# Optimization experiments

Hardware: AMD Instinct MI355X
Metric: run time of the kernel (lower is better)

The kernel has to match this reference:

```python
import jax, jax.numpy as jnp
import numpy as np

CLASS_NUM = 20
C_FEAT = 256
STRIDE = 16
ROI = 7
SCALE = 1.0 / 16.0
TOPK = 300
NMS_THR = 0.7
SCORE_THR = 0.5
SAMPLES = 2  # nearest samples per bin edge in roi_pool


def _conv(x, W, b, stride, padding):
    y = jax.lax.conv_general_dilated(x, W, (stride, stride), padding,
                                     dimension_numbers=('NCHW', 'OIHW', 'NCHW'))
    return y + b[None, :, None, None]


def _pairwise_iou(boxes):
    x1, y1, x2, y2 = boxes[:, 0], boxes[:, 1], boxes[:, 2], boxes[:, 3]
    area = jnp.maximum(x2 - x1, 0.) * jnp.maximum(y2 - y1, 0.)
    ix1 = jnp.maximum(x1[:, None], x1[None, :])
    iy1 = jnp.maximum(y1[:, None], y1[None, :])
    ix2 = jnp.minimum(x2[:, None], x2[None, :])
    iy2 = jnp.minimum(y2[:, None], y2[None, :])
    inter = jnp.maximum(ix2 - ix1, 0.) * jnp.maximum(iy2 - iy1, 0.)
    return inter / jnp.maximum(area[:, None] + area[None, :] - inter, 1e-6)


def _nms(boxes, scores, valid, thr):
    # fixed-size greedy NMS: returns boolean keep mask aligned with input order
    K = boxes.shape[0]
    order = jnp.argsort(-scores)
    b = boxes[order]
    v = valid[order]
    iou = _pairwise_iou(b)  # [K,K]
    idx = jnp.arange(K)

    def body(i, keep):
        k = keep[i] & v[i]
        suppress = (iou[i] > thr) & (idx > i) & k
        return keep & (~suppress)

    keep = jax.lax.fori_loop(0, K, body, v)
    return jnp.zeros((K,), bool).at[order].set(keep)


def _roi_pool(f, boxes):
    # f: [C,H,W] feature map; boxes: [K,4] in image coords.
    # Max pool over ROI x SAMPLES nearest-neighbor samples per bin (jit-safe roi_pool).
    C, H, W = f.shape
    K = boxes.shape[0]
    b = boxes * SCALE
    frac = (jnp.arange(ROI)[:, None] + (jnp.arange(SAMPLES)[None, :] + 0.5) / SAMPLES).reshape(-1) / ROI
    xs = b[:, 0:1] + frac[None, :] * (b[:, 2:3] - b[:, 0:1])  # [K, ROI*S]
    ys = b[:, 1:2] + frac[None, :] * (b[:, 3:4] - b[:, 1:2])
    ix = jnp.clip(jnp.floor(xs), 0, W - 1).astype(jnp.int32)
    iy = jnp.clip(jnp.floor(ys), 0, H - 1).astype(jnp.int32)
    g = f[:, iy[:, :, None], ix[:, None, :]]  # [C,K,ROI*S,ROI*S]
    g = g.reshape(C, K, ROI, SAMPLES, ROI, SAMPLES)
    return g.max(axis=(3, 5)).transpose(1, 0, 2, 3)  # [K,C,ROI,ROI]


def setup_inputs() -> dict:
    key = jax.random.key(0)
    ks = jax.random.split(key, 12)
    img = 800
    x = jax.random.uniform(ks[0], (1, 3, img, img), jnp.float32)
    gt_boxes = jax.random.uniform(ks[1], (8, 5), jnp.float32) * img

    def w_(k, shape, fan_in):
        return jax.random.normal(k, shape, jnp.float32) * (1.0 / np.sqrt(fan_in))

    d_flat = ROI * ROI * C_FEAT
    return {
        'x': x, 'gt_boxes': gt_boxes,
        'W_feat': w_(ks[2], (C_FEAT, 3, STRIDE, STRIDE), 3 * STRIDE * STRIDE),
        'b_feat': jnp.zeros((C_FEAT,), jnp.float32),
        'W1': w_(ks[3], (C_FEAT, C_FEAT, 3, 3), C_FEAT * 9),
        'b1': jnp.zeros((C_FEAT,), jnp.float32),
        'Wc': w_(ks[4], (2, C_FEAT), C_FEAT),
        'bc': jnp.zeros((2,), jnp.float32),
        'Wb': w_(ks[5], (4, C_FEAT), C_FEAT),
        'bb': jnp.zeros((4,), jnp.float32),
        'fc1_w': w_(ks[6], (4096, d_flat), d_flat),
        'fc1_b': jnp.zeros((4096,), jnp.float32),
        'fc2_w': w_(ks[7], (4096, 4096), 4096),
        'fc2_b': jnp.zeros((4096,), jnp.float32),
        'cls_w': w_(ks[8], (CLASS_NUM + 1, 4096), 4096),
        'cls_b': jnp.zeros((CLASS_NUM + 1,), jnp.float32),
        'box_w': w_(ks[9], (4, 4096), 4096),
        'box_b': jnp.zeros((4,), jnp.float32),
        'w': 800, 'h': 800,
    }


def reference(x, gt_boxes, W_feat, b_feat, W1, b1, Wc, bc, Wb, bb,
              fc1_w, fc1_b, fc2_w, fc2_b, cls_w, cls_b, box_w, box_b, w, h):
    feature = _conv(x, W_feat, b_feat, STRIDE, 'VALID')          # [1,C,50,50]
    hmap = jax.nn.relu(_conv(feature, W1, b1, 1, 'SAME'))
    pre_labels = (jnp.einsum('nchw,oc->nhwo', hmap, Wc) + bc).reshape(-1, 2)
    pre_boxes = (jnp.einsum('nchw,oc->nhwo', hmap, Wb) + bb).reshape(-1, 4)
    logits = jax.nn.softmax(pre_labels, axis=-1)[:, 1]           # [2500]
    scores, idx = jax.lax.top_k(logits, TOPK)                    # fixed-size stand-in for score>thr select
    valid = scores > SCORE_THR
    pb = pre_boxes[idx]
    wf = jnp.float32(w)
    hf = jnp.float32(h)
    # box decode exactly as the original per-box loop (vectorized)
    x1 = jnp.maximum(pb[:, 2] - pb[:, 0] / 2, 0.)
    y1 = jnp.maximum(pb[:, 3] - pb[:, 1] / 2, 0.)
    x2 = jnp.minimum(pb[:, 2] + pb[:, 0], wf)
    y2 = jnp.minimum(pb[:, 3] + pb[:, 1], hf)
    boxes = jnp.stack([x1, y1, x2, y2], axis=-1)                 # [K,4]
    keep = _nms(boxes, scores, valid, NMS_THR)
    pooled = _roi_pool(feature[0], boxes)                        # [K,C,7,7]
    flat = pooled.reshape(TOPK, -1)
    h1 = jax.nn.relu(flat @ fc1_w.T + fc1_b)
    h2 = jax.nn.relu(h1 @ fc2_w.T + fc2_b)
    cls = h2 @ cls_w.T + cls_b                                   # [K,21]
    box = h2 @ box_w.T + box_b                                   # [K,4]
    out = jnp.where(keep[:, None], jnp.concatenate([cls, box], axis=-1), 0.)
    return out                                                   # [K,25]
```

## Files before the change

kernel.cpp:

```cpp
#include <hip/hip_runtime.h>
#include <hip/hip_bf16.h>
#include <math.h>

#define NPIX   2500
#define CFEAT  256
#define NTOP   300
#define DFLAT  12544
#define FCN    4096
#define FPSTRIDE 3328
#define KG1    392
#define KG2    128
#define MT     20

typedef _Float16 f16x8 __attribute__((ext_vector_type(8)));
typedef float    f32x4 __attribute__((ext_vector_type(4)));

static constexpr size_t OFF_FPAD  = 0;
static constexpr size_t OFF_SCORE = 0x5C0000;
static constexpr size_t OFF_PREB  = 0x5D0000;
static constexpr size_t OFF_KEEP  = 0x5E5000;
static constexpr size_t OFF_IX    = 0x5E6000;
static constexpr size_t OFF_IY    = 0x5EB000;
static constexpr size_t OFF_AFRAG = 0x600000;
static constexpr size_t OFF_H1F   = 0xE00000;
static constexpr size_t OFF_H2    = 0x1100000;
static constexpr size_t OFF_W1T   = 0x1600000;
static constexpr size_t OFF_PART  = 0x1900000;

__device__ inline float decode_dim(const void* p) {
    int iv = *(const int*)p;
    if (iv > 0 && iv < (1 << 20)) return (float)iv;
    return __int_as_float(iv);
}

__global__ void zero_fpad(float* __restrict__ fpad) {
    int i = blockIdx.x * 256 + threadIdx.x;
    if (i < 212992) *(float4*)(fpad + (size_t)i * 4) = make_float4(0.f, 0.f, 0.f, 0.f);
}

__global__ void __launch_bounds__(256)
patch_conv(const float* __restrict__ x, const float* __restrict__ Wf,
           const float* __restrict__ bf, float* __restrict__ fpad) {
    __shared__ float w[3072];
    int co0 = blockIdx.y * 4;
    for (int t = threadIdx.x; t < 3072; t += 256) w[t] = Wf[co0 * 768 + t];
    __syncthreads();
    int p = blockIdx.x * 256 + threadIdx.x;
    if (p >= NPIX) return;
    int py = p / 50, px = p % 50;
    float acc[4];
    #pragma unroll
    for (int c = 0; c < 4; ++c) acc[c] = bf[co0 + c];
    for (int ci = 0; ci < 3; ++ci) {
        const float* xp = x + ci * 640000 + (py * 16) * 800 + px * 16;
        #pragma unroll
        for (int ky = 0; ky < 16; ++ky) {
            const float* row = xp + ky * 800;
            #pragma unroll
            for (int kq = 0; kq < 4; ++kq) {
                float4 xv = *reinterpret_cast<const float4*>(row + kq * 4);
                int kb = ci * 256 + ky * 16 + kq * 4;
                #pragma unroll
                for (int c = 0; c < 4; ++c) {
                    const float* wc = w + c * 768 + kb;
                    acc[c] += xv.x * wc[0] + xv.y * wc[1] + xv.z * wc[2] + xv.w * wc[3];
                }
            }
        }
    }
    size_t o = (size_t)(py + 1) * 64 + (px + 1);
    #pragma unroll
    for (int c = 0; c < 4; ++c) fpad[(size_t)(co0 + c) * FPSTRIDE + o] = acc[c];
}

__global__ void transpose_w1(const float* __restrict__ W1, float* __restrict__ W1t) {
    int idx = blockIdx.x * 256 + threadIdx.x;
    if (idx >= 2304 * 256) return;
    int r = idx >> 8, co = idx & 255;
    W1t[idx] = W1[co * 2304 + r];
}

__global__ void __launch_bounds__(256)
conv3x3_part(const float* __restrict__ fpad, const float* __restrict__ W1t,
             float* __restrict__ cpart, int zci) {
    int co = threadIdx.x;
    int xb = blockIdx.x * 8;
    int y  = blockIdx.y;
    int z  = blockIdx.z;
    float acc[8];
    #pragma unroll
    for (int p = 0; p < 8; ++p) acc[p] = 0.0f;
    const float* fp = fpad + (size_t)(z * zci) * FPSTRIDE + (size_t)y * 64 + xb;
    const float* wp = W1t + (size_t)(z * zci) * 9 * 256 + co;
    #pragma unroll 2
    for (int ci = 0; ci < zci; ++ci) {
        float v[3][12];
        #pragma unroll
        for (int dy = 0; dy < 3; ++dy) {
            #pragma unroll
            for (int q = 0; q < 3; ++q) {
                float4 r4 = *(const float4*)(fp + dy * 64 + q * 4);
                v[dy][q * 4 + 0] = r4.x; v[dy][q * 4 + 1] = r4.y;
                v[dy][q * 4 + 2] = r4.z; v[dy][q * 4 + 3] = r4.w;
            }
        }
        float wv[9];
        #pragma unroll
        for (int k = 0; k < 9; ++k) wv[k] = wp[k * 256];
        #pragma unroll
        for (int dy = 0; dy < 3; ++dy)
            #pragma unroll
            for (int dx = 0; dx < 3; ++dx) {
                float wvv = wv[dy * 3 + dx];
                #pragma unroll
                for (int p = 0; p < 8; ++p)
                    acc[p] += v[dy][p + dx] * wvv;
            }
        fp += FPSTRIDE;
        wp += 9 * 256;
    }
    size_t base = (size_t)z * (NPIX * 256) + (size_t)(y * 50 + xb) * 256 + co;
    #pragma unroll
    for (int p = 0; p < 8; ++p)
        if (xb + p < 50) cpart[base + (size_t)p * 256] = acc[p];
}

__global__ void __launch_bounds__(256)
reducehead_k(const float* __restrict__ cpart, const float* __restrict__ b1,
             const float* __restrict__ Wc, const float* __restrict__ bc,
             const float* __restrict__ Wb, const float* __restrict__ bb,
             float* __restrict__ score, float* __restrict__ preb, int zs) {
    int lane = threadIdx.x & 63;
    int p = blockIdx.x * 4 + (threadIdx.x >> 6);
    if (p >= NPIX) return;
    size_t off = (size_t)p * 256 + lane * 4;
    float4 h = *(const float4*)(cpart + off);
    for (int z = 1; z < zs; ++z) {
        float4 v = *(const float4*)(cpart + (size_t)z * (NPIX * 256) + off);
        h.x += v.x; h.y += v.y; h.z += v.z; h.w += v.w;
    }
    float4 b = *(const float4*)(b1 + lane * 4);
    h.x = fmaxf(h.x + b.x, 0.f); h.y = fmaxf(h.y + b.y, 0.f);
    h.z = fmaxf(h.z + b.z, 0.f); h.w = fmaxf(h.w + b.w, 0.f);
    float4 c0 = *(const float4*)(Wc + lane * 4);
    float4 c1 = *(const float4*)(Wc + 256 + lane * 4);
    float4 w0 = *(const float4*)(Wb + lane * 4);
    float4 w1 = *(const float4*)(Wb + 256 + lane * 4);
    float4 w2 = *(const float4*)(Wb + 512 + lane * 4);
    float4 w3 = *(const float4*)(Wb + 768 + lane * 4);
    float s[6];
    s[0] = h.x*c0.x + h.y*c0.y + h.z*c0.z + h.w*c0.w;
    s[1] = h.x*c1.x + h.y*c1.y + h.z*c1.z + h.w*c1.w;
    s[2] = h.x*w0.x + h.y*w0.y + h.z*w0.z + h.w*w0.w;
    s[3] = h.x*w1.x + h.y*w1.y + h.z*w1.z + h.w*w1.w;
    s[4] = h.x*w2.x + h.y*w2.y + h.z*w2.z + h.w*w2.w;
    s[5] = h.x*w3.x + h.y*w3.y + h.z*w3.z + h.w*w3.w;
    #pragma unroll
    for (int o = 1; o < 64; o <<= 1) {
        #pragma unroll
        for (int q = 0; q < 6; ++q) s[q] += __shfl_xor(s[q], o, 64);
    }
    if (lane == 0) {
        float s0 = s[0] + bc[0], s1 = s[1] + bc[1];
        float m = fmaxf(s0, s1);
        float e0 = expf(s0 - m), e1 = expf(s1 - m);
        score[p] = e1 / (e0 + e1);
        preb[p * 4 + 0] = s[2] + bb[0];
        preb[p * 4 + 1] = s[3] + bb[1];
        preb[p * 4 + 2] = s[4] + bb[2];
        preb[p * 4 + 3] = s[5] + bb[3];
    }
}

__global__ void __launch_bounds__(1024)
topknms_k(const float* __restrict__ score, const float* __restrict__ preb,
          const void* wp_, const void* hp_, int* __restrict__ keep,
          int* __restrict__ ixb, int* __restrict__ iyb) {
    __shared__ unsigned long long KEYS[NPIX];
    __shared__ unsigned int hist[256];
    __shared__ int sh_digit, sh_newr, cnt;
    __shared__ unsigned long long SEL[NTOP];
    __shared__ unsigned long long SORT[NTOP];
    __shared__ float X1[320], Y1[320], X2[320], Y2[320], AR[320];
    __shared__ unsigned long long MASK[320][5];
    __shared__ unsigned long long KEEPW[5];
    int tid = threadIdx.x;
    int lane = tid & 63;
    int w = tid >> 6;

    for (int e = tid; e < NPIX; e += 1024) {
        unsigned sb = __float_as_uint(score[e]);
        KEYS[e] = ((unsigned long long)sb << 32) | (unsigned)(~e);
    }
    if (tid == 0) cnt = 0;
    __syncthreads();

    unsigned long long P = 0ull, M = 0ull;
    int r = NTOP;
    for (int pass = 0; pass < 8; ++pass) {
        int shift = 56 - 8 * pass;
        if (tid < 256) hist[tid] = 0u;
        __syncthreads();
        for (int e = tid; e < NPIX; e += 1024) {
            unsigned long long k = KEYS[e];
            if ((k & M) == P)
                atomicAdd(&hist[(unsigned)(k >> shift) & 255u], 1u);
        }
        __syncthreads();
        if (tid < 64) {
            unsigned c0 = hist[tid * 4 + 0], c1 = hist[tid * 4 + 1];
            unsigned c2 = hist[tid * 4 + 2], c3 = hist[tid * 4 + 3];
            unsigned sl = c0 + c1 + c2 + c3;
            unsigned suf = sl;
            #pragma unroll
            for (int off = 1; off < 64; off <<= 1) {
                unsigned o = __shfl_down(suf, off, 64);
                if (lane + off < 64) suf += o;
            }
            unsigned G = suf - sl;
            if (G < (unsigned)r && G + sl >= (unsigned)r) {
                unsigned cc[4] = {c0, c1, c2, c3};
                int d = 0; unsigned ab = G;
                #pragma unroll
                for (int i = 3; i >= 0; --i) {
                    if (ab < (unsigned)r && ab + cc[i] >= (unsigned)r) { d = tid * 4 + i; break; }
                    ab += cc[i];
                }
                sh_digit = d;
                sh_newr = r - (int)ab;
            }
        }
        __syncthreads();
        P |= ((unsigned long long)(unsigned)sh_digit) << shift;
        M |= 0xFFull << shift;
        r = sh_newr;
    }
    unsigned long long T = P;

    for (int e = tid; e < NPIX; e += 1024) {
        unsigned long long k = KEYS[e];
        if (k >= T) {
            int s = atomicAdd(&cnt, 1);
            SEL[s] = k;
        }
    }
    __syncthreads();

    if (tid < NTOP) {
        unsigned long long mine = SEL[tid];
        int rank = 0;
        for (int j = 0; j < NTOP; ++j) rank += (SEL[j] > mine) ? 1 : 0;
        SORT[rank] = mine;
    }
    __syncthreads();

    if (tid < 320) {
        float x1 = 0.f, y1 = 0.f, x2 = 0.f, y2 = 0.f;
        bool v = false;
        if (tid < NTOP) {
            unsigned long long key = SORT[tid];
            int id = (int)(~(unsigned)key);
            float sc = __uint_as_float((unsigned)(key >> 32));
            float wf = decode_dim(wp_), hf = decode_dim(hp_);
            float p0 = preb[id * 4 + 0], p1 = preb[id * 4 + 1];
            float p2 = preb[id * 4 + 2], p3 = preb[id * 4 + 3];
            x1 = fmaxf(p2 - p0 * 0.5f, 0.0f);
            y1 = fmaxf(p3 - p1 * 0.5f, 0.0f);
            x2 = fminf(p2 + p0, wf);
            y2 = fminf(p3 + p1, hf);
            v = sc > 0.5f;
            float bx1 = x1 * 0.0625f, by1 = y1 * 0.0625f;
            float bx2 = x2 * 0.0625f, by2 = y2 * 0.0625f;
            #pragma unroll
            for (int m = 0; m < 14; ++m) {
                int i = m >> 1, s = m & 1;
                float frac = ((float)i + (s ? 0.75f : 0.25f)) / 7.0f;
                float xs = bx1 + frac * (bx2 - bx1);
                float ys = by1 + frac * (by2 - by1);
                float fx = floorf(xs); fx = fminf(fmaxf(fx, 0.0f), 49.0f);
                float fy = floorf(ys); fy = fminf(fmaxf(fy, 0.0f), 49.0f);
                ixb[tid * 14 + m] = (int)fx;
                iyb[tid * 14 + m] = (int)fy;
            }
        }
        X1[tid] = x1; Y1[tid] = y1; X2[tid] = x2; Y2[tid] = y2;
        AR[tid] = fmaxf(x2 - x1, 0.0f) * fmaxf(y2 - y1, 0.0f);
        unsigned long long vb = __ballot(v);
        if (lane == 0 && w < 5) KEEPW[w] = vb;
    }
    __syncthreads();

    if (tid < 320) {
        float xi1 = X1[tid], yi1 = Y1[tid], xi2 = X2[tid], yi2 = Y2[tid], ai = AR[tid];
        #pragma unroll
        for (int jw = 0; jw < 5; ++jw) {
            unsigned long long mword = 0ull;
            #pragma unroll 4
            for (int j2 = 0; j2 < 64; ++j2) {
                int j = jw * 64 + j2;
                float ix1 = fmaxf(xi1, X1[j]);
                float iy1 = fmaxf(yi1, Y1[j]);
                float ix2 = fminf(xi2, X2[j]);
                float iy2 = fminf(yi2, Y2[j]);
                float inter = fmaxf(ix2 - ix1, 0.0f) * fmaxf(iy2 - iy1, 0.0f);
                float iou = inter / fmaxf(ai + AR[j] - inter, 1e-6f);
                bool sup = (iou > 0.7f) && (j > tid) && (j < NTOP);
                mword |= sup ? (1ull << j2) : 0ull;
            }
            MASK[tid][jw] = mword;
        }
    }
    __syncthreads();

    if (tid < 64) {
        unsigned long long m[5][5];
        #pragma unroll
        for (int g = 0; g < 5; ++g)
            #pragma unroll
            for (int q = 0; q < 5; ++q)
                m[g][q] = MASK[g * 64 + lane][q];
        unsigned long long kw0 = KEEPW[0], kw1 = KEEPW[1], kw2 = KEEPW[2],
                           kw3 = KEEPW[3], kw4 = KEEPW[4];
        #pragma unroll
        for (int g = 0; g < 5; ++g) {
            for (int i2 = 0; i2 < 64; ++i2) {
                unsigned long long kg = (g == 0) ? kw0 : (g == 1) ? kw1 :
                                        (g == 2) ? kw2 : (g == 3) ? kw3 : kw4;
                bool alive = (kg >> i2) & 1ull;
                unsigned long long b0 = __shfl(m[g][0], i2, 64);
                unsigned long long b1 = __shfl(m[g][1], i2, 64);
                unsigned long long b2 = __shfl(m[g][2], i2, 64);
                unsigned long long b3 = __shfl(m[g][3], i2, 64);
                unsigned long long b4 = __shfl(m[g][4], i2, 64);
                if (alive) {
                    kw0 &= ~b0; kw1 &= ~b1; kw2 &= ~b2; kw3 &= ~b3; kw4 &= ~b4;
                }
            }
        }
        #pragma unroll
        for (int g = 0; g < 5; ++g) {
            unsigned long long kg = (g == 0) ? kw0 : (g == 1) ? kw1 :
                                    (g == 2) ? kw2 : (g == 3) ? kw3 : kw4;
            int j = g * 64 + lane;
            if (j < NTOP) keep[j] = (int)((kg >> lane) & 1ull);
        }
    }
}

__global__ void __launch_bounds__(256)
roipool_frag(const float* __restrict__ fpad, const int* __restrict__ ixb,
             const int* __restrict__ iyb, _Float16* __restrict__ Af) {
    int wid = blockIdx.x * 256 + threadIdx.x;
    if (wid >= MT * KG1 * 64) return;
    int l = wid & 63;
    int g = (wid >> 6) % KG1;
    int T = wid / (KG1 * 64);
    int mm = T * 16 + (l & 15);
    int kbase = g * 32 + ((l >> 4) & 3) * 8;
    union { _Float16 h[8]; uint4 u; } o;
    if (mm < NTOP) {
        const int* ix = ixb + mm * 14;
        const int* iy = iyb + mm * 14;
        #pragma unroll
        for (int e = 0; e < 8; ++e) {
            int k = kbase + e;
            int c = k / 49, ij = k % 49, i = ij / 7, jx = ij % 7;
            int y0 = iy[2 * i] + 1, y1 = iy[2 * i + 1] + 1;
            int x0 = ix[2 * jx] + 1, x1 = ix[2 * jx + 1] + 1;
            const float* f = fpad + (size_t)c * FPSTRIDE;
            float v = fmaxf(fmaxf(f[y0 * 64 + x0], f[y0 * 64 + x1]),
                            fmaxf(f[y1 * 64 + x0], f[y1 * 64 + x1]));
            o.h[e] = (_Float16)v;
        }
    } else {
        o.u.x = 0u; o.u.y = 0u; o.u.z = 0u; o.u.w = 0u;
    }
    *(uint4*)(Af + (size_t)wid * 8) = o.u;
}

__global__ void __launch_bounds__(1024)
gemm_fullm(const _Float16* __restrict__ Af, const float* __restrict__ B,
           float* __restrict__ part, int K, int KG, int kchunk, int ns) {
    __shared__ char Bs[2][128 * 128];
    int tid = threadIdx.x;
    int lane = tid & 63;
    int w = tid >> 6;
    int wm = w & 3, wn = w >> 2;
    int wg = blockIdx.x;
    int kz = wg % ns;
    int n0 = (wg / ns) * 128;
    int ks = kz * kchunk;
    int klen = K - ks; if (klen > kchunk) klen = kchunk;
    int nt = klen >> 6;

    f32x4 acc[5][2];
    #pragma unroll
    for (int tm = 0; tm < 5; ++tm)
        #pragma unroll
        for (int tn = 0; tn < 2; ++tn)
            acc[tm][tn] = f32x4{0.f, 0.f, 0.f, 0.f};

    int srow = tid >> 3;
    int skp  = (tid & 7) * 8;
    const float* bsrc = B + (size_t)(n0 + srow) * K + ks + skp;
    int sboff = srow * 128 + ((skp * 2) ^ ((srow & 7) << 4));

    float4 v0 = *(const float4*)(bsrc);
    float4 v1 = *(const float4*)(bsrc + 4);
    {
        union { _Float16 h[8]; uint4 u; } cv;
        cv.h[0] = (_Float16)v0.x; cv.h[1] = (_Float16)v0.y;
        cv.h[2] = (_Float16)v0.z; cv.h[3] = (_Float16)v0.w;
        cv.h[4] = (_Float16)v1.x; cv.h[5] = (_Float16)v1.y;
        cv.h[6] = (_Float16)v1.z; cv.h[7] = (_Float16)v1.w;
        *(uint4*)(Bs[0] + sboff) = cv.u;
    }
    if (nt > 1) {
        v0 = *(const float4*)(bsrc + 64);
        v1 = *(const float4*)(bsrc + 68);
    }
    __syncthreads();

    for (int k0 = 0; k0 < nt; ++k0) {
        const char* cur = Bs[k0 & 1];
        if (k0 + 1 < nt) {
            union { _Float16 h[8]; uint4 u; } cv;
            cv.h[0] = (_Float16)v0.x; cv.h[1] = (_Float16)v0.y;
            cv.h[2] = (_Float16)v0.z; cv.h[3] = (_Float16)v0.w;
            cv.h[4] = (_Float16)v1.x; cv.h[5] = (_Float16)v1.y;
            cv.h[6] = (_Float16)v1.z; cv.h[7] = (_Float16)v1.w;
            *(uint4*)(Bs[(k0 + 1) & 1] + sboff) = cv.u;
            if (k0 + 2 < nt) {
                v0 = *(const float4*)(bsrc + (k0 + 2) * 64);
                v1 = *(const float4*)(bsrc + (k0 + 2) * 64 + 4);
            }
        }
        int g0 = (ks + k0 * 64) >> 5;
        f16x8 a0[5], a1[5];
        #pragma unroll
        for (int tm = 0; tm < 5; ++tm) {
            int T = wm * 5 + tm;
            a0[tm] = *(const f16x8*)(Af + ((size_t)(T * KG + g0) * 64 + lane) * 8);
            a1[tm] = *(const f16x8*)(Af + ((size_t)(T * KG + g0 + 1) * 64 + lane) * 8);
        }
        f16x8 b0[2], b1[2];
        #pragma unroll
        for (int tn = 0; tn < 2; ++tn) {
            int row = wn * 32 + tn * 16 + (lane & 15);
            int kb0 = (lane >> 4) * 16;
            b0[tn] = *(const f16x8*)(cur + row * 128 + (kb0 ^ ((row & 7) << 4)));
            b1[tn] = *(const f16x8*)(cur + row * 128 + ((kb0 + 64) ^ ((row & 7) << 4)));
        }
        #pragma unroll
        for (int tm = 0; tm < 5; ++tm)
            #pragma unroll
            for (int tn = 0; tn < 2; ++tn) {
                acc[tm][tn] = __builtin_amdgcn_mfma_f32_16x16x32_f16(a0[tm], b0[tn], acc[tm][tn], 0, 0, 0);
                acc[tm][tn] = __builtin_amdgcn_mfma_f32_16x16x32_f16(a1[tm], b1[tn], acc[tm][tn], 0, 0, 0);
            }
        __syncthreads();
    }
    float* pout = part + (size_t)kz * (NTOP * FCN);
    #pragma unroll
    for (int tm = 0; tm < 5; ++tm) {
        int mbase = (wm * 5 + tm) * 16 + (lane >> 4) * 4;
        #pragma unroll
        for (int j = 0; j < 4; ++j) {
            int m = mbase + j;
            if (m < NTOP) {
                #pragma unroll
                for (int tn = 0; tn < 2; ++tn) {
                    int n = n0 + wn * 32 + tn * 16 + (lane & 15);
                    pout[(size_t)m * FCN + n] = acc[tm][tn][j];
                }
            }
        }
    }
}

__global__ void reduce_fc1(const float* __restrict__ part, const float* __restrict__ bias,
                           _Float16* __restrict__ h1f, int ns) {
    int i = blockIdx.x * 256 + threadIdx.x;
    if (i >= NTOP * 512) return;
    int m = i >> 9;
    int f = (i & 511) * 8;
    float s[8];
    const float* p0 = part + (size_t)m * FCN + f;
    #pragma unroll
    for (int e = 0; e < 8; ++e) s[e] = p0[e];
    for (int z = 1; z < ns; ++z) {
        const float* pz = p0 + (size_t)z * (NTOP * FCN);
        #pragma unroll
        for (int e = 0; e < 8; ++e) s[e] += pz[e];
    }
    union { _Float16 h[8]; uint4 u; } o;
    #pragma unroll
    for (int e = 0; e < 8; ++e) o.h[e] = (_Float16)fmaxf(s[e] + bias[f + e], 0.0f);
    int T = m >> 4, g = f >> 5, l = (m & 15) + 16 * ((f >> 3) & 3);
    *(uint4*)(h1f + ((size_t)(T * KG2 + g) * 64 + l) * 8) = o.u;
}

__global__ void reduce_fc2(const float* __restrict__ part, const float* __restrict__ bias,
                           float* __restrict__ outp, int ns) {
    size_t i = (size_t)blockIdx.x * 256 + threadIdx.x;
    size_t mn4 = (size_t)NTOP * FCN / 4;
    if (i >= mn4) return;
    float4 s = *(const float4*)(part + i * 4);
    for (int zz = 1; zz < ns; ++zz) {
        float4 v = *(const float4*)(part + (size_t)zz * (NTOP * FCN) + i * 4);
        s.x += v.x; s.y += v.y; s.z += v.z; s.w += v.w;
    }
    int n = (int)((i * 4) % FCN);
    float4 b = *(const float4*)(bias + n);
    s.x = fmaxf(s.x + b.x, 0.f); s.y = fmaxf(s.y + b.y, 0.f);
    s.z = fmaxf(s.z + b.z, 0.f); s.w = fmaxf(s.w + b.w, 0.f);
    *(float4*)(outp + i * 4) = s;
}

__global__ void __launch_bounds__(256)
final_k(const float* __restrict__ h2, const float* __restrict__ clsw,
        const float* __restrict__ clsb, const float* __restrict__ boxw,
        const float* __restrict__ boxb, const int* __restrict__ keep,
        float* __restrict__ out) {
    int gid = blockIdx.x * 4 + (threadIdx.x >> 6);
    if (gid >= NTOP * 25) return;
    int lane = threadIdx.x & 63;
    int k = gid / 25, o = gid % 25;
    const float* w;
    float b;
    if (o < 21) { w = clsw + (size_t)o * 4096; b = clsb[o]; }
    else        { w = boxw + (size_t)(o - 21) * 4096; b = boxb[o - 21]; }
    const float* h = h2 + (size_t)k * 4096;
    float s = 0.0f;
    #pragma unroll
    for (int i = 0; i < 16; ++i) {
        float4 hv = *(const float4*)(h + (i * 64 + lane) * 4);
        float4 wv = *(const float4*)(w + (i * 64 + lane) * 4);
        s += hv.x * wv.x + hv.y * wv.y + hv.z * wv.z + hv.w * wv.w;
    }
    #pragma unroll
    for (int off = 1; off < 64; off <<= 1) s += __shfl_xor(s, off, 64);
    if (lane == 0) out[gid] = keep[k] ? (s + b) : 0.0f;
}

extern "C" void kernel_launch(void* const* d_in, const int* in_sizes, int n_in,
                              void* d_out, int out_size, void* d_ws, size_t ws_size,
                              hipStream_t stream) {
    const float* x    = (const float*)d_in[0];
    const float* Wf   = (const float*)d_in[2];
    const float* bf   = (const float*)d_in[3];
    const float* W1   = (const float*)d_in[4];
    const float* b1   = (const float*)d_in[5];
    const float* Wc   = (const float*)d_in[6];
    const float* bc   = (const float*)d_in[7];
    const float* Wb   = (const float*)d_in[8];
    const float* bb   = (const float*)d_in[9];
    const float* fc1w = (const float*)d_in[10];
    const float* fc1b = (const float*)d_in[11];
    const float* fc2w = (const float*)d_in[12];
    const float* fc2b = (const float*)d_in[13];
    const float* clsw = (const float*)d_in[14];
    const float* clsb = (const float*)d_in[15];
    const float* boxw = (const float*)d_in[16];
    const float* boxb = (const float*)d_in[17];
    const void*  wp   = d_in[18];
    const void*  hp   = d_in[19];

    char* ws = (char*)d_ws;
    float*     fpad  = (float*)(ws + OFF_FPAD);
    float*     score = (float*)(ws + OFF_SCORE);
    float*     preb  = (float*)(ws + OFF_PREB);
    int*       keep  = (int*)(ws + OFF_KEEP);
    int*       ixb   = (int*)(ws + OFF_IX);
    int*       iyb   = (int*)(ws + OFF_IY);
    _Float16*  Af    = (_Float16*)(ws + OFF_AFRAG);
    _Float16*  h1f   = (_Float16*)(ws + OFF_H1F);
    float*     h2    = (float*)(ws + OFF_H2);
    float*     w1t   = (float*)(ws + OFF_W1T);
    float*     out   = (float*)d_out;

    size_t slot = (size_t)NTOP * FCN * 4;
    size_t avail = ws_size > OFF_PART ? (ws_size - OFF_PART) / slot : 0;
    int ns1 = (avail >= 8) ? 8 : (avail >= 4) ? 4 : (avail >= 2) ? 2 : 1;
    int ns2 = ns1;
    float* part1 = (avail >= 1) ? (float*)(ws + OFF_PART) : h2;
    float* part2 = (avail >= 1) ? (float*)(ws + OFF_PART) : (float*)Af;
    int st1 = (196 + ns1 - 1) / ns1;  int kch1 = st1 * 64;  int ns1e = (196 + st1 - 1) / st1;
    int st2 = (64 + ns2 - 1) / ns2;   int kch2 = st2 * 64;  int ns2e = (64 + st2 - 1) / st2;
    int zs = (avail >= 5) ? 8 : 4;
    float* cpart = (avail >= 5) ? (float*)(ws + OFF_PART) : (float*)(ws + OFF_AFRAG);

    zero_fpad<<<832, 256, 0, stream>>>(fpad);
    patch_conv<<<dim3(10, 64), 256, 0, stream>>>(x, Wf, bf, fpad);
    transpose_w1<<<(2304 * 256 + 255) / 256, 256, 0, stream>>>(W1, w1t);
    conv3x3_part<<<dim3(7, 50, zs), 256, 0, stream>>>(fpad, w1t, cpart, 256 / zs);
    reducehead_k<<<625, 256, 0, stream>>>(cpart, b1, Wc, bc, Wb, bb, score, preb, zs);
    topknms_k<<<1, 1024, 0, stream>>>(score, preb, wp, hp, keep, ixb, iyb);
    roipool_frag<<<(MT * KG1 * 64 + 255) / 256, 256, 0, stream>>>(fpad, ixb, iyb, Af);
    gemm_fullm<<<32 * ns1e, 1024, 0, stream>>>(Af, fc1w, part1, DFLAT, KG1, kch1, ns1e);
    reduce_fc1<<<(NTOP * 512 + 255) / 256, 256, 0, stream>>>(part1, fc1b, h1f, ns1e);
    gemm_fullm<<<32 * ns2e, 1024, 0, stream>>>(h1f, fc2w, part2, FCN, KG2, kch2, ns2e);
    reduce_fc2<<<(NTOP * FCN / 4 + 255) / 256, 256, 0, stream>>>(part2, fc2b, h2, ns2e);
    final_k<<<(NTOP * 25 + 3) / 4, 256, 0, stream>>>(h2, clsw, clsb, boxw, boxb, keep, out);
}
```

Baseline: 345.9 us.

## Merge prep kernels, use per-wave radix histograms, shrink GEMM tiles to 64 columns

Fuses the fpad zeroing and W1 transpose into one launch so there is one fewer kernel. The top-k radix pass now keeps a separate histogram per wave, which cuts shared-memory atomic contention and removes one barrier per pass, at the cost of a 16-way reduction. The FC GEMMs switch to 512-thread blocks with 64-wide N tiles and twice as many blocks, with a launch bound asking for 4 blocks per CU. The inner loop is also reordered to load A and B fragments one k-half at a time, which lowers register pressure. The GEMM changes may be incomplete: the B-tile load indexing and the warp mapping (wn up to 1 with 8 waves) must match the halved tile size.

Measured after the change: 342.9 us. No clear change (-0.9%).

```diff
diff --git a/kernel.cpp b/kernel.cpp
--- a/kernel.cpp
+++ b/kernel.cpp
@@ -33,9 +33,19 @@
     return __int_as_float(iv);
 }
 
-__global__ void zero_fpad(float* __restrict__ fpad) {
-    int i = blockIdx.x * 256 + threadIdx.x;
-    if (i < 212992) *(float4*)(fpad + (size_t)i * 4) = make_float4(0.f, 0.f, 0.f, 0.f);
+__global__ void prep_k(float* __restrict__ fpad, const float* __restrict__ W1,
+                       float* __restrict__ W1t) {
+    int b = blockIdx.x;
+    if (b < 832) {
+        int i = b * 256 + threadIdx.x;
+        if (i < 212992) *(float4*)(fpad + (size_t)i * 4) = make_float4(0.f, 0.f, 0.f, 0.f);
+    } else {
+        int idx = (b - 832) * 256 + threadIdx.x;
+        if (idx < 2304 * 256) {
+            int r = idx >> 8, co = idx & 255;
+            W1t[idx] = W1[co * 2304 + r];
+        }
+    }
 }
 
 __global__ void __launch_bounds__(256)
@@ -71,13 +81,6 @@
     size_t o = (size_t)(py + 1) * 64 + (px + 1);
     #pragma unroll
     for (int c = 0; c < 4; ++c) fpad[(size_t)(co0 + c) * FPSTRIDE + o] = acc[c];
-}
-
-__global__ void transpose_w1(const float* __restrict__ W1, float* __restrict__ W1t) {
-    int idx = blockIdx.x * 256 + threadIdx.x;
-    if (idx >= 2304 * 256) return;
-    int r = idx >> 8, co = idx & 255;
-    W1t[idx] = W1[co * 2304 + r];
 }
 
 __global__ void __launch_bounds__(256)
@@ -177,7 +180,7 @@
           const void* wp_, const void* hp_, int* __restrict__ keep,
           int* __restrict__ ixb, int* __restrict__ iyb) {
     __shared__ unsigned long long KEYS[NPIX];
-    __shared__ unsigned int hist[256];
+    __shared__ unsigned int whist[16][256];
     __shared__ int sh_digit, sh_newr, cnt;
     __shared__ unsigned long long SEL[NTOP];
     __shared__ unsigned long long SORT[NTOP];
@@ -199,17 +202,22 @@
     int r = NTOP;
     for (int pass = 0; pass < 8; ++pass) {
         int shift = 56 - 8 * pass;
-        if (tid < 256) hist[tid] = 0u;
-        __syncthreads();
+        *(uint4*)&whist[w][lane * 4] = uint4{0u, 0u, 0u, 0u};
         for (int e = tid; e < NPIX; e += 1024) {
             unsigned long long k = KEYS[e];
             if ((k & M) == P)
-                atomicAdd(&hist[(unsigned)(k >> shift) & 255u], 1u);
+                atomicAdd(&whist[w][(unsigned)(k >> shift) & 255u], 1u);
         }
         __syncthreads();
         if (tid < 64) {
-            unsigned c0 = hist[tid * 4 + 0], c1 = hist[tid * 4 + 1];
-            unsigned c2 = hist[tid * 4 + 2], c3 = hist[tid * 4 + 3];
+            unsigned c0 = 0, c1 = 0, c2 = 0, c3 = 0;
+            #pragma unroll
+            for (int ww = 0; ww < 16; ++ww) {
+                c0 += whist[ww][tid * 4 + 0];
+                c1 += whist[ww][tid * 4 + 1];
+                c2 += whist[ww][tid * 4 + 2];
+                c3 += whist[ww][tid * 4 + 3];
+            }
             unsigned sl = c0 + c1 + c2 + c3;
             unsigned suf = sl;
             #pragma unroll
@@ -378,17 +386,17 @@
     *(uint4*)(Af + (size_t)wid * 8) = o.u;
 }
 
-__global__ void __launch_bounds__(1024)
+__global__ void __launch_bounds__(512, 4)
 gemm_fullm(const _Float16* __restrict__ Af, const float* __restrict__ B,
            float* __restrict__ part, int K, int KG, int kchunk, int ns) {
-    __shared__ char Bs[2][128 * 128];
+    __shared__ char Bs[2][64 * 128];
     int tid = threadIdx.x;
     int lane = tid & 63;
     int w = tid >> 6;
     int wm = w & 3, wn = w >> 2;
     int wg = blockIdx.x;
     int kz = wg % ns;
-    int n0 = (wg / ns) * 128;
+    int n0 = (wg / ns) * 64;
     int ks = kz * kchunk;
     int klen = K - ks; if (klen > kchunk) klen = kchunk;
     int nt = klen >> 6;
@@ -436,28 +444,27 @@
             }
         }
         int g0 = (ks + k0 * 64) >> 5;
-        f16x8 a0[5], a1[5];
-        #pragma unroll
-        for (int tm = 0; tm < 5; ++tm) {
-            int T = wm * 5 + tm;
-            a0[tm] = *(const f16x8*)(Af + ((size_t)(T * KG + g0) * 64 + lane) * 8);
-            a1[tm] = *(const f16x8*)(Af + ((size_t)(T * KG + g0 + 1) * 64 + lane) * 8);
-        }
-        f16x8 b0[2], b1[2];
-        #pragma unroll
-        for (int tn = 0; tn < 2; ++tn) {
-            int row = wn * 32 + tn * 16 + (lane & 15);
-            int kb0 = (lane >> 4) * 16;
-            b0[tn] = *(const f16x8*)(cur + row * 128 + (kb0 ^ ((row & 7) << 4)));
-            b1[tn] = *(const f16x8*)(cur + row * 128 + ((kb0 + 64) ^ ((row & 7) << 4)));
-        }
-        #pragma unroll
-        for (int tm = 0; tm < 5; ++tm)
+        #pragma unroll
+        for (int kk = 0; kk < 2; ++kk) {
+            f16x8 bfr[2];
             #pragma unroll
             for (int tn = 0; tn < 2; ++tn) {
-                acc[tm][tn] = __builtin_amdgcn_mfma_f32_16x16x32_f16(a0[tm], b0[tn], acc[tm][tn], 0, 0, 0);
-                acc[tm][tn] = __builtin_amdgcn_mfma_f32_16x16x32_f16(a1[tm], b1[tn], acc[tm][tn], 0, 0, 0);
-            }
+                int row = wn * 32 + tn * 16 + (lane & 15);
+                int kb = kk * 64 + (lane >> 4) * 16;
+                bfr[tn] = *(const f16x8*)(cur + row * 128 + (kb ^ ((row & 7) << 4)));
+            }
+            f16x8 a[5];
+            #pragma unroll
+            for (int tm = 0; tm < 5; ++tm) {
+                int T = wm * 5 + tm;
+                a[tm] = *(const f16x8*)(Af + ((size_t)(T * KG + g0 + kk) * 64 + lane) * 8);
+            }
+            #pragma unroll
+            for (int tm = 0; tm < 5; ++tm)
+                #pragma unroll
+                for (int tn = 0; tn < 2; ++tn)
+                    acc[tm][tn] = __builtin_amdgcn_mfma_f32_16x16x32_f16(a[tm], bfr[tn], acc[tm][tn], 0, 0, 0);
+        }
         __syncthreads();
     }
     float* pout = part + (size_t)kz * (NTOP * FCN);
@@ -590,16 +597,15 @@
     int zs = (avail >= 5) ? 8 : 4;
     float* cpart = (avail >= 5) ? (float*)(ws + OFF_PART) : (float*)(ws + OFF_AFRAG);
 
-    zero_fpad<<<832, 256, 0, stream>>>(fpad);
+    prep_k<<<832 + 2304, 256, 0, stream>>>(fpad, W1, w1t);
     patch_conv<<<dim3(10, 64), 256, 0, stream>>>(x, Wf, bf, fpad);
-    transpose_w1<<<(2304 * 256 + 255) / 256, 256, 0, stream>>>(W1, w1t);
     conv3x3_part<<<dim3(7, 50, zs), 256, 0, stream>>>(fpad, w1t, cpart, 256 / zs);
     reducehead_k<<<625, 256, 0, stream>>>(cpart, b1, Wc, bc, Wb, bb, score, preb, zs);
     topknms_k<<<1, 1024, 0, stream>>>(score, preb, wp, hp, keep, ixb, iyb);
     roipool_frag<<<(MT * KG1 * 64 + 255) / 256, 256, 0, stream>>>(fpad, ixb, iyb, Af);
-    gemm_fullm<<<32 * ns1e, 1024, 0, stream>>>(Af, fc1w, part1, DFLAT, KG1, kch1, ns1e);
+    gemm_fullm<<<64 * ns1e, 512, 0, stream>>>(Af, fc1w, part1, DFLAT, KG1, kch1, ns1e);
     reduce_fc1<<<(NTOP * 512 + 255) / 256, 256, 0, stream>>>(part1, fc1b, h1f, ns1e);
-    gemm_fullm<<<32 * ns2e, 1024, 0, stream>>>(h1f, fc2w, part2, FCN, KG2, kch2, ns2e);
+    gemm_fullm<<<64 * ns2e, 512, 0, stream>>>(h1f, fc2w, part2, FCN, KG2, kch2, ns2e);
     reduce_fc2<<<(NTOP * FCN / 4 + 255) / 256, 256, 0, stream>>>(part2, fc2b, h2, ns2e);
     final_k<<<(NTOP * 25 + 3) / 4, 256, 0, stream>>>(h2, clsw, clsb, boxw, boxb, keep, out);
 }
```
